# Optimization experiments

Measured on AMD Instinct MI355X. Metric: run time of the kernel, lower is better.

Reference implementation:

```python
import jax, jax.numpy as jnp
import numpy as np

LN_EPS = 1e-5


def setup_inputs() -> dict:
    key = jax.random.key(0)
    ks = jax.random.split(key, 5)
    L, G, D, E = 2, 50000, 128, 800000
    x = jax.random.normal(ks[0], (L, G, D), dtype=jnp.float32)
    rows = jax.random.randint(ks[1], (E,), 0, G, dtype=jnp.int32)
    cols = jax.random.randint(ks[2], (E,), 0, G, dtype=jnp.int32)
    vals = jax.random.uniform(ks[3], (E,), dtype=jnp.float32)
    W = jax.random.normal(ks[4], (D, D), dtype=jnp.float32) * 0.05
    b = jnp.zeros((D,), dtype=jnp.float32)
    gamma = jnp.ones((D,), dtype=jnp.float32)
    beta = jnp.zeros((D,), dtype=jnp.float32)
    return {"x": x, "rows": rows, "cols": cols, "vals": vals,
            "W": W, "b": b, "gamma": gamma, "beta": beta}


def reference(x, rows, cols, vals, W, b, gamma, beta):
    L, G, D = x.shape
    # sparse connection_matrix @ x, edge-list form (COO): out[r] += v * x_t[c]
    xt = x.transpose(1, 0, 2).reshape(G, L * D)          # [G, L*D]
    msg = xt[cols] * vals[:, None]                        # [E, L*D]
    agg = jax.ops.segment_sum(msg, rows, num_segments=G)  # [G, L*D]
    y = agg.reshape(G, L, D).transpose(1, 0, 2)           # [L, G, D]
    # linear + SiLU
    h = jnp.einsum('lgd,od->lgo', y, W) + b
    s = h * jax.nn.sigmoid(h)
    # LayerNorm over last dim
    mu = jnp.mean(s, axis=-1, keepdims=True)
    var = jnp.mean(jnp.square(s - mu), axis=-1, keepdims=True)
    out = (s - mu) * jax.lax.rsqrt(var + LN_EPS) * gamma + beta
    return out
```

## Files before the change

### kernel.cpp

```cpp
#include <hip/hip_runtime.h>
#include <hip/hip_bf16.h>
#include <math.h>

typedef short bf16x8 __attribute__((ext_vector_type(8)));
typedef float f32x4 __attribute__((ext_vector_type(4)));

#define SPW 2
#define CAP 64

static __device__ __forceinline__ float bf2f(ushort u) {
  union { unsigned i; float f; } c;
  c.i = ((unsigned)u) << 16;
  return c.f;
}

static __device__ __forceinline__ ushort f2bf(float f) {
  __hip_bfloat16 h = __float2bfloat16(f);
  return *reinterpret_cast<ushort*>(&h);
}

__global__ __launch_bounds__(256) void zgemm_bucket_kernel(
    const float* __restrict__ x, const float* __restrict__ W,
    ushort* __restrict__ zb, int nstripes, int nz,
    const int* __restrict__ rows, const int* __restrict__ cols,
    const float* __restrict__ vals, int* __restrict__ counts,
    int2* __restrict__ ev, int E) {
  if ((int)blockIdx.x >= nz) {
    int e = ((int)blockIdx.x - nz) * 256 + threadIdx.x;
    if (e >= E) return;
    int r = rows[e];
    int pos = atomicAdd(&counts[r], 1);
    if (pos < CAP)
      ev[(size_t)r * CAP + pos] =
          make_int2(cols[e] << 8, __float_as_int(vals[e]));
    return;
  }

  const int lane = threadIdx.x & 63;
  const int wid = blockIdx.x * 4 + (threadIdx.x >> 6);

  const int o_lo = lane & 15;
  const int kg = lane >> 4;

  bf16x8 wf[8][4];
#pragma unroll
  for (int on = 0; on < 8; ++on)
#pragma unroll
    for (int kc = 0; kc < 4; ++kc) {
      const float* src = W + (size_t)(on * 16 + o_lo) * 128 + kc * 32 + kg * 8;
      float4 v0 = *reinterpret_cast<const float4*>(src);
      float4 v1 = *reinterpret_cast<const float4*>(src + 4);
      bf16x8 t;
      t[0] = (short)f2bf(v0.x); t[1] = (short)f2bf(v0.y);
      t[2] = (short)f2bf(v0.z); t[3] = (short)f2bf(v0.w);
      t[4] = (short)f2bf(v1.x); t[5] = (short)f2bf(v1.y);
      t[6] = (short)f2bf(v1.z); t[7] = (short)f2bf(v1.w);
      wf[on][kc] = t;
    }

  for (int i = 0; i < SPW; ++i) {
    const int s = wid * SPW + i;
    if (s >= nstripes) return;
    const int row0 = s << 4;

    bf16x8 af[4];
#pragma unroll
    for (int kc = 0; kc < 4; ++kc) {
      const float* src = x + (size_t)(row0 + o_lo) * 128 + kc * 32 + kg * 8;
      float4 v0 = *reinterpret_cast<const float4*>(src);
      float4 v1 = *reinterpret_cast<const float4*>(src + 4);
      bf16x8 t;
      t[0] = (short)f2bf(v0.x); t[1] = (short)f2bf(v0.y);
      t[2] = (short)f2bf(v0.z); t[3] = (short)f2bf(v0.w);
      t[4] = (short)f2bf(v1.x); t[5] = (short)f2bf(v1.y);
      t[6] = (short)f2bf(v1.z); t[7] = (short)f2bf(v1.w);
      af[kc] = t;
    }

    f32x4 acc[8];
#pragma unroll
    for (int on = 0; on < 8; ++on) acc[on] = (f32x4){0.f, 0.f, 0.f, 0.f};

#pragma unroll
    for (int kc = 0; kc < 4; ++kc)
#pragma unroll
      for (int on = 0; on < 8; ++on)
        acc[on] = __builtin_amdgcn_mfma_f32_16x16x32_bf16(af[kc], wf[on][kc],
                                                          acc[on], 0, 0, 0);

#pragma unroll
    for (int reg = 0; reg < 4; ++reg) {
      ushort* zr = zb + (size_t)(row0 + kg * 4 + reg) * 128 + o_lo;
#pragma unroll
      for (int on = 0; on < 8; ++on) zr[on * 16] = f2bf(acc[on][reg]);
    }
  }
}

__global__ __launch_bounds__(256) void gather_fused_kernel(
    const ushort* __restrict__ zb, const int* __restrict__ counts,
    const int2* __restrict__ ev, const float* __restrict__ b,
    const float* __restrict__ gamma, const float* __restrict__ beta,
    float* __restrict__ out, int G, int GD) {
  int g = blockIdx.x * 4 + (threadIdx.x >> 6);
  if (g >= G) return;
  const int lane = threadIdx.x & 63;
  const int l = lane >> 5;
  const int q = lane & 31;
  const char* zbase = (const char*)(zb + (size_t)l * GD);
  const uint qoff = (uint)q << 3;

  const int2* evr = ev + (size_t)g * CAP;
  int n = counts[g];
  if (n > CAP) n = CAP;
  float4 acc = make_float4(0.f, 0.f, 0.f, 0.f);

  int i = 0;
  for (; i + 3 < n; i += 4) {
    int2 e0 = evr[i], e1 = evr[i + 1], e2 = evr[i + 2], e3 = evr[i + 3];
    ushort4 a0 = *reinterpret_cast<const ushort4*>(zbase + ((uint)e0.x + qoff));
    ushort4 a1 = *reinterpret_cast<const ushort4*>(zbase + ((uint)e1.x + qoff));
    ushort4 a2 = *reinterpret_cast<const ushort4*>(zbase + ((uint)e2.x + qoff));
    ushort4 a3 = *reinterpret_cast<const ushort4*>(zbase + ((uint)e3.x + qoff));
    float v0 = __int_as_float(e0.y), v1 = __int_as_float(e1.y);
    float v2 = __int_as_float(e2.y), v3 = __int_as_float(e3.y);
    acc.x += v0 * bf2f(a0.x) + v1 * bf2f(a1.x) + v2 * bf2f(a2.x) + v3 * bf2f(a3.x);
    acc.y += v0 * bf2f(a0.y) + v1 * bf2f(a1.y) + v2 * bf2f(a2.y) + v3 * bf2f(a3.y);
    acc.z += v0 * bf2f(a0.z) + v1 * bf2f(a1.z) + v2 * bf2f(a2.z) + v3 * bf2f(a3.z);
    acc.w += v0 * bf2f(a0.w) + v1 * bf2f(a1.w) + v2 * bf2f(a2.w) + v3 * bf2f(a3.w);
  }
  for (; i < n; ++i) {
    int2 e0 = evr[i];
    float v0 = __int_as_float(e0.y);
    ushort4 a0 = *reinterpret_cast<const ushort4*>(zbase + ((uint)e0.x + qoff));
    acc.x += v0 * bf2f(a0.x);
    acc.y += v0 * bf2f(a0.y);
    acc.z += v0 * bf2f(a0.z);
    acc.w += v0 * bf2f(a0.w);
  }

  const int d0 = q * 4;
  const float4 bb = *reinterpret_cast<const float4*>(b + d0);
  float4 s;
  {
    float h0 = acc.x + bb.x, h1 = acc.y + bb.y;
    float h2 = acc.z + bb.z, h3 = acc.w + bb.w;
    s.x = h0 / (1.f + expf(-h0));
    s.y = h1 / (1.f + expf(-h1));
    s.z = h2 / (1.f + expf(-h2));
    s.w = h3 / (1.f + expf(-h3));
  }
  float sum = s.x + s.y + s.z + s.w;
  float sq = s.x * s.x + s.y * s.y + s.z * s.z + s.w * s.w;
#pragma unroll
  for (int m = 1; m <= 16; m <<= 1) {
    sum += __shfl_xor(sum, m);
    sq += __shfl_xor(sq, m);
  }
  const float mu = sum * (1.f / 128.f);
  const float var = sq * (1.f / 128.f) - mu * mu;
  const float inv = rsqrtf(var + 1e-5f);
  const float4 gm = *reinterpret_cast<const float4*>(gamma + d0);
  const float4 bt = *reinterpret_cast<const float4*>(beta + d0);
  float4 o;
  o.x = (s.x - mu) * inv * gm.x + bt.x;
  o.y = (s.y - mu) * inv * gm.y + bt.y;
  o.z = (s.z - mu) * inv * gm.z + bt.z;
  o.w = (s.w - mu) * inv * gm.w + bt.w;
  *reinterpret_cast<float4*>(out + (size_t)l * GD + (size_t)g * 128 + d0) = o;
}

extern "C" void kernel_launch(void* const* d_in, const int* in_sizes, int n_in,
                              void* d_out, int out_size, void* d_ws,
                              size_t ws_size, hipStream_t stream) {
  const float* x = (const float*)d_in[0];
  const int* rows = (const int*)d_in[1];
  const int* cols = (const int*)d_in[2];
  const float* vals = (const float*)d_in[3];
  const float* W = (const float*)d_in[4];
  const float* b = (const float*)d_in[5];
  const float* gamma = (const float*)d_in[6];
  const float* beta = (const float*)d_in[7];

  const int E = in_sizes[1];
  const int G = in_sizes[0] / 256;
  const int GD = G * 128;

  char* ws = (char*)d_ws;
  ushort* zb = (ushort*)ws;
  int* counts = (int*)(zb + (size_t)2 * GD);
  int* counts_end = counts + G + (G & 1);
  int2* ev = (int2*)counts_end;

  (void)hipMemsetAsync(counts, 0, (size_t)G * sizeof(int), stream);

  const int nstripes = (G * 2) / 16;
  const int nz = (nstripes + 4 * SPW - 1) / (4 * SPW);
  const int nbk = (E + 255) / 256;
  zgemm_bucket_kernel<<<nz + nbk, 256, 0, stream>>>(
      x, W, zb, nstripes, nz, rows, cols, vals, counts, ev, E);
  gather_fused_kernel<<<(G + 3) / 4, 256, 0, stream>>>(zb, counts, ev, b,
                                                       gamma, beta,
                                                       (float*)d_out, G, GD);
}
```

Measured before the change: 152.3 us.

## Pre-convert W to bf16, stream weight fragments, interleave GEMM and bucketing blocks

Adds a prep kernel that converts W to bf16 once and zeroes the counts array, which replaces the memset. The GEMM blocks now load bf16 weight fragments from global/L2 inside the MFMA loop instead of holding 32 converted fragments in registers, and launch bounds ask for higher occupancy. GEMM blocks are interleaved 1-in-3 with edge-bucketing blocks, and each bucketing thread handles two edges with vectorized loads. This trades register pressure and repeated per-block W conversion for extra cached weight loads in the inner loop and one additional kernel launch.

```diff
diff --git a/kernel.cpp b/kernel.cpp
--- a/kernel.cpp
+++ b/kernel.cpp
@@ -19,49 +19,63 @@
   return *reinterpret_cast<ushort*>(&h);
 }
 
-__global__ __launch_bounds__(256) void zgemm_bucket_kernel(
-    const float* __restrict__ x, const float* __restrict__ W,
+__global__ __launch_bounds__(256) void prep_kernel(const float* __restrict__ W,
+                                                   ushort* __restrict__ Wb,
+                                                   int* __restrict__ counts,
+                                                   int G) {
+  int t = blockIdx.x * 256 + threadIdx.x;
+  if (t < 16384) Wb[t] = f2bf(W[t]);
+  for (int i = t; i < G; i += (int)gridDim.x * 256) counts[i] = 0;
+}
+
+__global__ __launch_bounds__(256, 6) void zgemm_bucket_kernel(
+    const float* __restrict__ x, const ushort* __restrict__ Wb,
     ushort* __restrict__ zb, int nstripes, int nz,
     const int* __restrict__ rows, const int* __restrict__ cols,
     const float* __restrict__ vals, int* __restrict__ counts,
     int2* __restrict__ ev, int E) {
-  if ((int)blockIdx.x >= nz) {
-    int e = ((int)blockIdx.x - nz) * 256 + threadIdx.x;
-    if (e >= E) return;
-    int r = rows[e];
-    int pos = atomicAdd(&counts[r], 1);
-    if (pos < CAP)
-      ev[(size_t)r * CAP + pos] =
-          make_int2(cols[e] << 8, __float_as_int(vals[e]));
+  const int bid = blockIdx.x;
+  const bool isz = (bid % 3 == 0) && (bid / 3 < nz);
+
+  if (!isz) {
+    const int nzbefore = min((bid + 2) / 3, nz);
+    const int bi = bid - nzbefore;
+    const int e = (bi * 256 + (int)threadIdx.x) * 2;
+    if (e + 1 < E) {
+      const int2 r2 = *reinterpret_cast<const int2*>(rows + e);
+      const int2 c2 = *reinterpret_cast<const int2*>(cols + e);
+      const float2 v2 = *reinterpret_cast<const float2*>(vals + e);
+      int p0 = atomicAdd(&counts[r2.x], 1);
+      int p1 = atomicAdd(&counts[r2.y], 1);
+      if (p0 < CAP)
+        ev[(size_t)r2.x * CAP + p0] = make_int2(c2.x << 8, __float_as_int(v2.x));
+      if (p1 < CAP)
+        ev[(size_t)r2.y * CAP + p1] = make_int2(c2.y << 8, __float_as_int(v2.y));
+    } else if (e < E) {
+      int r = rows[e];
+      int pos = atomicAdd(&counts[r], 1);
+      if (pos < CAP)
+        ev[(size_t)r * CAP + pos] =
+            make_int2(cols[e] << 8, __float_as_int(vals[e]));
+    }
     return;
   }
 
+  const int zi = bid / 3;
   const int lane = threadIdx.x & 63;
-  const int wid = blockIdx.x * 4 + (threadIdx.x >> 6);
+  const int wid = zi * 4 + (threadIdx.x >> 6);
 
   const int o_lo = lane & 15;
   const int kg = lane >> 4;
-
-  bf16x8 wf[8][4];
-#pragma unroll
-  for (int on = 0; on < 8; ++on)
-#pragma unroll
-    for (int kc = 0; kc < 4; ++kc) {
-      const float* src = W + (size_t)(on * 16 + o_lo) * 128 + kc * 32 + kg * 8;
-      float4 v0 = *reinterpret_cast<const float4*>(src);
-      float4 v1 = *reinterpret_cast<const float4*>(src + 4);
-      bf16x8 t;
-      t[0] = (short)f2bf(v0.x); t[1] = (short)f2bf(v0.y);
-      t[2] = (short)f2bf(v0.z); t[3] = (short)f2bf(v0.w);
-      t[4] = (short)f2bf(v1.x); t[5] = (short)f2bf(v1.y);
-      t[6] = (short)f2bf(v1.z); t[7] = (short)f2bf(v1.w);
-      wf[on][kc] = t;
-    }
+  const ushort* wbp = Wb + o_lo * 128 + kg * 8;
 
   for (int i = 0; i < SPW; ++i) {
     const int s = wid * SPW + i;
     if (s >= nstripes) return;
     const int row0 = s << 4;
+
+    const ushort* wcur = wbp;
+    asm volatile("" : "+v"(wcur));
 
     bf16x8 af[4];
 #pragma unroll
@@ -84,9 +98,12 @@
 #pragma unroll
     for (int kc = 0; kc < 4; ++kc)
 #pragma unroll
-      for (int on = 0; on < 8; ++on)
-        acc[on] = __builtin_amdgcn_mfma_f32_16x16x32_bf16(af[kc], wf[on][kc],
+      for (int on = 0; on < 8; ++on) {
+        const bf16x8 wf =
+            *reinterpret_cast<const bf16x8*>(wcur + on * 2048 + kc * 32);
+        acc[on] = __builtin_amdgcn_mfma_f32_16x16x32_bf16(af[kc], wf,
                                                           acc[on], 0, 0, 0);
+      }
 
 #pragma unroll
     for (int reg = 0; reg < 4; ++reg) {
@@ -189,16 +206,16 @@
   char* ws = (char*)d_ws;
   ushort* zb = (ushort*)ws;
   int* counts = (int*)(zb + (size_t)2 * GD);
-  int* counts_end = counts + G + (G & 1);
-  int2* ev = (int2*)counts_end;
-
-  (void)hipMemsetAsync(counts, 0, (size_t)G * sizeof(int), stream);
+  ushort* Wb = (ushort*)(counts + G + (G & 1));
+  int2* ev = (int2*)(Wb + 16384);
+
+  prep_kernel<<<256, 256, 0, stream>>>(W, Wb, counts, G);
 
   const int nstripes = (G * 2) / 16;
   const int nz = (nstripes + 4 * SPW - 1) / (4 * SPW);
-  const int nbk = (E + 255) / 256;
+  const int nbk = (E / 2 + 255) / 256 + ((E & 1) ? 1 : 0);
   zgemm_bucket_kernel<<<nz + nbk, 256, 0, stream>>>(
-      x, W, zb, nstripes, nz, rows, cols, vals, counts, ev, E);
+      x, Wb, zb, nstripes, nz, rows, cols, vals, counts, ev, E);
   gather_fused_kernel<<<(G + 3) / 4, 256, 0, stream>>>(zb, counts, ev, b,
                                                        gamma, beta,
                                                        (float*)d_out, G, GD);
```

Result: slower. 161.0 us (+5.7%).
